# Optimization experiments

Hardware: AMD Instinct MI355X
Metric: run time of the kernel (lower is better)

## Reference

```python
import jax, jax.numpy as jnp
import numpy as np

BITS = 4
GROUP = 128
IN_F = 4096
OUT_F = 4096
N_TOK = 8192
N_STAGES = 4
QMAX = 2 ** BITS - 1  # affine (sym=False)


def _round_ste(x):
    return x + jax.lax.stop_gradient(jnp.round(x) - x)


def _clamp_ste(x, lo, hi):
    return x + jax.lax.stop_gradient(jnp.clip(x, lo, hi) - x)


def apply_rotation(x, pairs, theta, group_size):
    # x: [N, H]; pairs: [R, H] int (per-group index pairs in [0, group_size));
    # theta: [R, H//2]
    n, h = x.shape
    g = h // group_size
    half = group_size // 2
    offsets = (jnp.arange(g, dtype=jnp.int32) * group_size)[:, None]  # [G,1]
    pair_view = pairs.reshape(pairs.shape[0], g, half, 2)
    theta_view = theta.reshape(theta.shape[0], g, half)
    out = x
    for r in range(pairs.shape[0]):  # small fixed number of rotation stages
        idx_i = (pair_view[r, :, :, 0] + offsets).reshape(-1)  # [H//2]
        idx_j = (pair_view[r, :, :, 1] + offsets).reshape(-1)
        xi = out[:, idx_i]  # [N, H//2]
        xj = out[:, idx_j]
        c = jnp.cos(theta_view[r]).reshape(-1)[None, :]
        s = jnp.sin(theta_view[r]).reshape(-1)[None, :]
        out = out.at[:, idx_i].set(xi * c + xj * s).at[:, idx_j].set(-xi * s + xj * c)
    return out


def quant_dequant_affine_ste(w, scale, zero_point_float, group_size):
    # pseudo_quantize_dequant with sym=False, use_ste=True
    view = w.reshape(-1, group_size)
    s = _clamp_ste(scale, 1e-5, 1e5)
    rzp = _clamp_ste(-_round_ste(zero_point_float), 0.0, float(QMAX))
    q = _round_ste(view / s) + rzp
    q = _clamp_ste(q, 0.0, float(QMAX))
    return ((q - rzp) * s).reshape(w.shape)


def setup_inputs() -> dict:
    key = jax.random.key(0)
    k1, k2, k3, k4 = jax.random.split(key, 4)
    x = jax.random.normal(k1, (N_TOK, IN_F), dtype=jnp.float32)
    weight = jax.random.normal(k2, (OUT_F, IN_F), dtype=jnp.float32) * 0.02
    bias = jax.random.normal(k3, (OUT_F,), dtype=jnp.float32) * 0.01
    channel_scales = jnp.ones((IN_F,), dtype=jnp.float32)
    theta = jax.random.normal(k4, (N_STAGES, IN_F // 2), dtype=jnp.float32) * 0.05
    # per-group pair permutations: each stage/group is a permutation of [0, GROUP)
    rng = np.random.default_rng(0)
    g = IN_F // GROUP
    pairs_np = np.stack([
        np.concatenate([rng.permutation(GROUP) for _ in range(g)])
        for _ in range(N_STAGES)
    ]).astype(np.int32)  # [R, IN_F]
    pairs = jnp.asarray(pairs_np)
    # affine qparams from initial (theta=0, scales=1) transformed weight == weight
    view = weight.reshape(-1, GROUP)
    min_val = view.min(axis=1, keepdims=True)
    max_val = view.max(axis=1, keepdims=True)
    q_scale = jnp.clip(max_val - min_val, 1e-5, None) / QMAX
    q_zero_point = min_val / q_scale
    theta_mask = jnp.ones((N_STAGES, IN_F // 2), dtype=bool)
    return {"x": x, "weight": weight, "bias": bias,
            "channel_scales": channel_scales, "theta": theta,
            "q_scale": q_scale, "q_zero_point": q_zero_point,
            "pairs": pairs, "theta_mask": theta_mask}


def reference(x, weight, bias, channel_scales, theta, q_scale, q_zero_point, pairs, theta_mask):
    # transformed_weight(): scale input channels then group-wise Givens rotate
    w_scaled = weight * channel_scales[None, :]
    w_t = apply_rotation(w_scaled, pairs, theta, GROUP)
    # STE pseudo quantize-dequantize in the transformed domain
    w_q = quant_dequant_affine_ste(w_t, q_scale, q_zero_point, GROUP)
    # inverse rotation back to the original input domain, undo channel scales
    w_back = apply_rotation(w_q, pairs[::-1], -theta[::-1], GROUP) / channel_scales[None, :]
    return x @ w_back.T + bias[None, :]
```

## Files before the change

### kernel.cpp

```cpp
#include <hip/hip_runtime.h>
#include <hip/hip_bf16.h>
#include <math.h>

#define IN_F    4096
#define OUT_F   4096
#define N_TOK   8192
#define GROUP   128
#define NSTAGE  4
#define NPAIRS  2048
#define QMAXF   15.0

typedef unsigned short u16;
typedef __bf16 bf16x8 __attribute__((ext_vector_type(8)));
typedef float  f32x4  __attribute__((ext_vector_type(4)));

struct alignas(8) U16x4 { u16 x, y, z, w; };

__device__ __forceinline__ u16 f2bf(float f) {
    unsigned u = __float_as_uint(f);
    unsigned r = (u + 0x7fffu + ((u >> 16) & 1u)) >> 16;
    return (u16)r;
}

__device__ __forceinline__ void gl_lds16(const void* g, void* l) {
    __builtin_amdgcn_global_load_lds(
        (const __attribute__((address_space(1))) void*)g,
        (__attribute__((address_space(3))) void*)l,
        16, 0, 0);
}

__global__ void make_tabs(const float* __restrict__ theta,
                          double* __restrict__ ctab, double* __restrict__ stab) {
    int i = blockIdx.x * 256 + threadIdx.x;
    if (i < NSTAGE * NPAIRS) {
        double t = (double)theta[i];
        ctab[i] = cos(t);
        stab[i] = sin(t);
    }
}

__global__ __launch_bounds__(256) void build_w(
    const float* __restrict__ weight, const float* __restrict__ cs,
    const float* __restrict__ qs, const float* __restrict__ qzp,
    const int* __restrict__ pairs,
    const double* __restrict__ ctab, const double* __restrict__ stab,
    u16* __restrict__ wb) {
    __shared__ double gbuf[4][GROUP];
    const int wave = threadIdx.x >> 6, l = threadIdx.x & 63;
    const int task = blockIdx.x * 4 + wave;
    const int o = task >> 5, g = task & 31;
    double* gb = gbuf[wave];
    const int e0 = g * GROUP;

    float2 wv = *(const float2*)(weight + (size_t)o * IN_F + e0 + 2 * l);
    float2 cv = *(const float2*)(cs + e0 + 2 * l);
    gb[2 * l]     = (double)wv.x * (double)cv.x;
    gb[2 * l + 1] = (double)wv.y * (double)cv.y;
    __builtin_amdgcn_wave_barrier();

    const int2* prs = (const int2*)pairs;

    for (int r = 0; r < NSTAGE; ++r) {
        int2 p = prs[r * (IN_F / 2) + g * 64 + l];
        double c = ctab[r * NPAIRS + g * 64 + l];
        double s = stab[r * NPAIRS + g * 64 + l];
        double xi = gb[p.x], xj = gb[p.y];
        __builtin_amdgcn_wave_barrier();
        gb[p.x] =  xi * c + xj * s;
        gb[p.y] = -xi * s + xj * c;
        __builtin_amdgcn_wave_barrier();
    }

    {
        double s   = fmin(fmax((double)qs[o * 32 + g], 1e-5), 1e5);
        double rzp = fmin(fmax(-rint((double)qzp[o * 32 + g]), 0.0), QMAXF);
#pragma unroll
        for (int e = 2 * l; e <= 2 * l + 1; ++e) {
            double q = rint(gb[e] / s) + rzp;
            q = fmin(fmax(q, 0.0), QMAXF);
            gb[e] = (q - rzp) * s;
        }
        __builtin_amdgcn_wave_barrier();
    }

    for (int r = NSTAGE - 1; r >= 0; --r) {
        int2 p = prs[r * (IN_F / 2) + g * 64 + l];
        double c = ctab[r * NPAIRS + g * 64 + l];
        double s = stab[r * NPAIRS + g * 64 + l];
        double xi = gb[p.x], xj = gb[p.y];
        __builtin_amdgcn_wave_barrier();
        gb[p.x] = xi * c - xj * s;
        gb[p.y] = xi * s + xj * c;
        __builtin_amdgcn_wave_barrier();
    }

    unsigned lo = f2bf((float)(gb[2 * l]     / (double)cv.x));
    unsigned hi = f2bf((float)(gb[2 * l + 1] / (double)cv.y));
    *(unsigned*)(wb + (size_t)o * IN_F + e0 + 2 * l) = lo | (hi << 16);
}

__global__ void cast_x(const float* __restrict__ x, u16* __restrict__ xb) {
    size_t i = ((size_t)blockIdx.x * 256 + threadIdx.x) * 4;
    float4 v = *(const float4*)(x + i);
    U16x4 o;
    o.x = f2bf(v.x); o.y = f2bf(v.y); o.z = f2bf(v.z); o.w = f2bf(v.w);
    *(U16x4*)(xb + i) = o;
}

__global__ __launch_bounds__(512, 2) void gemm_bt(
    const u16* __restrict__ A, const u16* __restrict__ B,
    const float* __restrict__ bias, float* __restrict__ C) {
    constexpr int K = IN_F;
    constexpr int N = OUT_F;
    constexpr int NS = K / 32;
    __shared__ __align__(16) u16 As[4][256 * 32];
    __shared__ __align__(16) u16 Bs[4][256 * 32];

    const int tid  = threadIdx.x;
    const int wave = tid >> 6, lane = tid & 63;
    const int lrow = lane & 15, lq = lane >> 4;
    const int wm = wave >> 2, wn = wave & 3;

    const int wg = (blockIdx.x & 7) * 64 + (blockIdx.x >> 3);
    const int mt = wg & 31, nt = wg >> 5;
    const int m0 = mt * 256, n0 = nt * 256;

    const int srow = tid >> 2;
    const int gch  = (tid & 3) ^ ((tid >> 3) & 3);
    const u16* pA0 = A + (size_t)(m0 + srow) * K + gch * 8;
    const u16* pA1 = pA0 + (size_t)128 * K;
    const u16* pB0 = B + (size_t)(n0 + srow) * K + gch * 8;
    const u16* pB1 = pB0 + (size_t)128 * K;

#define STAGE(slot, s) do {                                         \
        const int ko_ = (s) * 32;                                   \
        gl_lds16(pA0 + ko_, &As[slot][wave * 512]);                 \
        gl_lds16(pA1 + ko_, &As[slot][4096 + wave * 512]);          \
        gl_lds16(pB0 + ko_, &Bs[slot][wave * 512]);                 \
        gl_lds16(pB1 + ko_, &Bs[slot][4096 + wave * 512]);          \
    } while (0)

    f32x4 acc[8][4];
#pragma unroll
    for (int i = 0; i < 8; ++i)
#pragma unroll
        for (int j = 0; j < 4; ++j) acc[i][j] = (f32x4){0.f, 0.f, 0.f, 0.f};

    STAGE(0, 0); STAGE(1, 1); STAGE(2, 2);

#define BODY(s, VMSTR, DO_STAGE) do {                                          \
        asm volatile("s_waitcnt " VMSTR);                                      \
        __builtin_amdgcn_s_barrier();                                          \
        asm volatile("" ::: "memory");                                         \
        const u16* as_ = As[(s) & 3];                                          \
        const u16* bs_ = Bs[(s) & 3];                                          \
        bf16x8 af[8], bf[4];                                                   \
        _Pragma("unroll")                                                      \
        for (int mi = 0; mi < 8; ++mi) {                                       \
            int ar = wm * 128 + mi * 16 + lrow;                                \
            af[mi] = *(const bf16x8*)&as_[ar * 32 +                            \
                                          (((lq ^ (ar >> 1)) & 3) << 3)];      \
        }                                                                      \
        _Pragma("unroll")                                                      \
        for (int nj = 0; nj < 4; ++nj) {                                       \
            int br = wn * 64 + nj * 16 + lrow;                                 \
            bf[nj] = *(const bf16x8*)&bs_[br * 32 +                            \
                                          (((lq ^ (br >> 1)) & 3) << 3)];      \
        }                                                                      \
        if (DO_STAGE) STAGE(((s) + 3) & 3, (s) + 3);                           \
        __builtin_amdgcn_s_setprio(1);                                         \
        _Pragma("unroll")                                                      \
        for (int mi = 0; mi < 8; ++mi)                                         \
            _Pragma("unroll")                                                  \
            for (int nj = 0; nj < 4; ++nj)                                     \
                acc[mi][nj] = __builtin_amdgcn_mfma_f32_16x16x32_bf16(         \
                    af[mi], bf[nj], acc[mi][nj], 0, 0, 0);                     \
        __builtin_amdgcn_s_setprio(0);                                         \
        asm volatile("" ::: "memory");                                         \
    } while (0)

    for (int s = 0; s < NS - 3; ++s)
        BODY(s, "vmcnt(8)", 1);
    BODY(NS - 3, "vmcnt(8)", 0);
    BODY(NS - 2, "vmcnt(4)", 0);
    BODY(NS - 1, "vmcnt(0)", 0);

#undef BODY
#undef STAGE

#pragma unroll
    for (int mi = 0; mi < 8; ++mi) {
        int rb = m0 + wm * 128 + mi * 16 + lq * 4;
#pragma unroll
        for (int nj = 0; nj < 4; ++nj) {
            int col = n0 + wn * 64 + nj * 16 + lrow;
            float bv = bias[col];
#pragma unroll
            for (int r = 0; r < 4; ++r)
                C[(size_t)(rb + r) * N + col] = acc[mi][nj][r] + bv;
        }
    }
}

extern "C" void kernel_launch(void* const* d_in, const int* in_sizes, int n_in,
                              void* d_out, int out_size, void* d_ws, size_t ws_size,
                              hipStream_t stream) {
    const float* x    = (const float*)d_in[0];
    const float* w    = (const float*)d_in[1];
    const float* bias = (const float*)d_in[2];
    const float* cs   = (const float*)d_in[3];
    const float* th   = (const float*)d_in[4];
    const float* qs   = (const float*)d_in[5];
    const float* qzp  = (const float*)d_in[6];
    const int*   pr   = (const int*)d_in[7];
    float* out = (float*)d_out;

    char* ws = (char*)d_ws;
    double* ctab = (double*)ws;
    double* stab = (double*)(ws + 65536);
    u16*    xb   = (u16*)(ws + 131072);
    u16*    wb   = (u16*)(ws + 131072 + (size_t)N_TOK * IN_F * 2);

    hipLaunchKernelGGL(make_tabs, dim3((NSTAGE * NPAIRS + 255) / 256), dim3(256),
                       0, stream, th, ctab, stab);
    hipLaunchKernelGGL(build_w, dim3(OUT_F * 32 / 4), dim3(256), 0, stream,
                       w, cs, qs, qzp, pr, ctab, stab, wb);
    hipLaunchKernelGGL(cast_x, dim3(N_TOK * IN_F / 4 / 256), dim3(256), 0, stream,
                       x, xb);
    hipLaunchKernelGGL(gemm_bt, dim3((N_TOK / 256) * (OUT_F / 256)), dim3(512),
                       0, stream, xb, wb, bias, out);
}
```

Baseline: 634.9 us.

## Restructure GEMM main loop into 64-wide K tiles with interleaved ping-pong phases

The bf16 GEMM now stages 256x64 K-tiles in a double-buffered LDS layout with an 8-way XOR swizzle, replacing the 4-deep 32-wide ring. Each K-group is split into four phases that alternate LDS fragment reads and MFMA bursts, separated by barriers. Global-to-LDS loads for A and B are issued at different phases so memory traffic overlaps compute. This aims to cut per-iteration barrier and waitcnt overhead and to schedule waves in a ping-pong pattern. In exchange there are many more barriers per tile and a shallower prefetch depth, which risks stalls.

```diff
diff --git a/kernel.cpp b/kernel.cpp
--- a/kernel.cpp
+++ b/kernel.cpp
@@ -27,6 +27,12 @@
         (const __attribute__((address_space(1))) void*)g,
         (__attribute__((address_space(3))) void*)l,
         16, 0, 0);
+}
+
+__device__ __forceinline__ void bar() {
+    asm volatile("" ::: "memory");
+    __builtin_amdgcn_s_barrier();
+    asm volatile("" ::: "memory");
 }
 
 __global__ void make_tabs(const float* __restrict__ theta,
@@ -112,9 +118,10 @@
     const float* __restrict__ bias, float* __restrict__ C) {
     constexpr int K = IN_F;
     constexpr int N = OUT_F;
-    constexpr int NS = K / 32;
-    __shared__ __align__(16) u16 As[4][256 * 32];
-    __shared__ __align__(16) u16 Bs[4][256 * 32];
+    constexpr int NGRP = K / 64;
+    constexpr int TIL = 256 * 64;
+    __shared__ __align__(16) u16 As[2][TIL];
+    __shared__ __align__(16) u16 Bs[2][TIL];
 
     const int tid  = threadIdx.x;
     const int wave = tid >> 6, lane = tid & 63;
@@ -125,19 +132,54 @@
     const int mt = wg & 31, nt = wg >> 5;
     const int m0 = mt * 256, n0 = nt * 256;
 
-    const int srow = tid >> 2;
-    const int gch  = (tid & 3) ^ ((tid >> 3) & 3);
-    const u16* pA0 = A + (size_t)(m0 + srow) * K + gch * 8;
-    const u16* pA1 = pA0 + (size_t)128 * K;
-    const u16* pB0 = B + (size_t)(n0 + srow) * K + gch * 8;
-    const u16* pB1 = pB0 + (size_t)128 * K;
-
-#define STAGE(slot, s) do {                                         \
-        const int ko_ = (s) * 32;                                   \
-        gl_lds16(pA0 + ko_, &As[slot][wave * 512]);                 \
-        gl_lds16(pA1 + ko_, &As[slot][4096 + wave * 512]);          \
-        gl_lds16(pB0 + ko_, &Bs[slot][wave * 512]);                 \
-        gl_lds16(pB1 + ko_, &Bs[slot][4096 + wave * 512]);          \
+    const int prow = tid >> 3;
+    const int pch  = (tid & 7) ^ ((tid >> 3) & 7);
+    const u16* pA = A + (size_t)(m0 + prow) * K + pch * 8;
+    const u16* pB = B + (size_t)(n0 + prow) * K + pch * 8;
+
+#define STAGE_A(slot, t) do {                                                  \
+        _Pragma("unroll")                                                      \
+        for (int hr_ = 0; hr_ < 4; ++hr_) {                                    \
+            const int h_ = hr_ >> 1, r_ = hr_ & 1;                             \
+            gl_lds16(pA + (size_t)(h_ * 128 + r_ * 64) * K + (t) * 64,         \
+                     &As[slot][h_ * 8192 + r_ * 4096 + (wave << 9)]);          \
+        }                                                                      \
+    } while (0)
+#define STAGE_B(slot, t) do {                                                  \
+        _Pragma("unroll")                                                      \
+        for (int hr_ = 0; hr_ < 4; ++hr_) {                                    \
+            const int h_ = hr_ >> 1, r_ = hr_ & 1;                             \
+            gl_lds16(pB + (size_t)(h_ * 128 + r_ * 64) * K + (t) * 64,         \
+                     &Bs[slot][h_ * 8192 + r_ * 4096 + (wave << 9)]);          \
+        }                                                                      \
+    } while (0)
+
+#define RD_A(ks) do {                                                          \
+        _Pragma("unroll")                                                      \
+        for (int mi_ = 0; mi_ < 8; ++mi_) {                                    \
+            const int ar_ = (wm << 7) + (mi_ << 4) + lrow;                     \
+            af[mi_] = *(const bf16x8*)&as_[(ar_ << 6) +                        \
+                (((((ks) << 2) | lq) ^ (ar_ & 7)) << 3)];                      \
+        }                                                                      \
+    } while (0)
+#define RD_B(ks, nj0) do {                                                     \
+        const int br0_ = (wn << 6) + ((nj0) << 4) + lrow;                      \
+        b0 = *(const bf16x8*)&bs_[(br0_ << 6) +                                \
+                (((((ks) << 2) | lq) ^ (br0_ & 7)) << 3)];                     \
+        b1 = *(const bf16x8*)&bs_[((br0_ + 16) << 6) +                         \
+                (((((ks) << 2) | lq) ^ (br0_ & 7)) << 3)];                     \
+    } while (0)
+
+#define MF2(nj0) do {                                                          \
+        __builtin_amdgcn_s_setprio(1);                                         \
+        _Pragma("unroll")                                                      \
+        for (int mi_ = 0; mi_ < 8; ++mi_) {                                    \
+            acc[mi_][nj0] = __builtin_amdgcn_mfma_f32_16x16x32_bf16(           \
+                af[mi_], b0, acc[mi_][nj0], 0, 0, 0);                          \
+            acc[mi_][(nj0) + 1] = __builtin_amdgcn_mfma_f32_16x16x32_bf16(     \
+                af[mi_], b1, acc[mi_][(nj0) + 1], 0, 0, 0);                    \
+        }                                                                      \
+        __builtin_amdgcn_s_setprio(0);                                         \
     } while (0)
 
     f32x4 acc[8][4];
@@ -146,47 +188,52 @@
 #pragma unroll
         for (int j = 0; j < 4; ++j) acc[i][j] = (f32x4){0.f, 0.f, 0.f, 0.f};
 
-    STAGE(0, 0); STAGE(1, 1); STAGE(2, 2);
-
-#define BODY(s, VMSTR, DO_STAGE) do {                                          \
-        asm volatile("s_waitcnt " VMSTR);                                      \
-        __builtin_amdgcn_s_barrier();                                          \
-        asm volatile("" ::: "memory");                                         \
-        const u16* as_ = As[(s) & 3];                                          \
-        const u16* bs_ = Bs[(s) & 3];                                          \
-        bf16x8 af[8], bf[4];                                                   \
-        _Pragma("unroll")                                                      \
-        for (int mi = 0; mi < 8; ++mi) {                                       \
-            int ar = wm * 128 + mi * 16 + lrow;                                \
-            af[mi] = *(const bf16x8*)&as_[ar * 32 +                            \
-                                          (((lq ^ (ar >> 1)) & 3) << 3)];      \
-        }                                                                      \
-        _Pragma("unroll")                                                      \
-        for (int nj = 0; nj < 4; ++nj) {                                       \
-            int br = wn * 64 + nj * 16 + lrow;                                 \
-            bf[nj] = *(const bf16x8*)&bs_[br * 32 +                            \
-                                          (((lq ^ (br >> 1)) & 3) << 3)];      \
-        }                                                                      \
-        if (DO_STAGE) STAGE(((s) + 3) & 3, (s) + 3);                           \
-        __builtin_amdgcn_s_setprio(1);                                         \
-        _Pragma("unroll")                                                      \
-        for (int mi = 0; mi < 8; ++mi)                                         \
-            _Pragma("unroll")                                                  \
-            for (int nj = 0; nj < 4; ++nj)                                     \
-                acc[mi][nj] = __builtin_amdgcn_mfma_f32_16x16x32_bf16(         \
-                    af[mi], bf[nj], acc[mi][nj], 0, 0, 0);                     \
-        __builtin_amdgcn_s_setprio(0);                                         \
-        asm volatile("" ::: "memory");                                         \
-    } while (0)
-
-    for (int s = 0; s < NS - 3; ++s)
-        BODY(s, "vmcnt(8)", 1);
-    BODY(NS - 3, "vmcnt(8)", 0);
-    BODY(NS - 2, "vmcnt(4)", 0);
-    BODY(NS - 1, "vmcnt(0)", 0);
-
-#undef BODY
-#undef STAGE
+    STAGE_A(0, 0); STAGE_B(0, 0); STAGE_A(1, 1); STAGE_B(1, 1);
+    asm volatile("s_waitcnt vmcnt(8)" ::: "memory");
+    __builtin_amdgcn_s_barrier();
+    asm volatile("" ::: "memory");
+
+#pragma unroll 2
+    for (int g = 0; g < NGRP; ++g) {
+        u16* as_ = As[g & 1];
+        u16* bs_ = Bs[g & 1];
+        bf16x8 af[8], b0, b1;
+
+        RD_A(0);
+        RD_B(0, 0);
+        if (g >= 1 && g + 1 < NGRP) STAGE_B((g + 1) & 1, g + 1);
+        bar();
+        MF2(0);
+        bar();
+
+        RD_B(0, 2);
+        bar();
+        MF2(2);
+        bar();
+
+        RD_A(1);
+        RD_B(1, 0);
+        bar();
+        MF2(0);
+        bar();
+
+        RD_B(1, 2);
+        if (g + 2 < NGRP) {
+            STAGE_A(g & 1, g + 2);
+            asm volatile("s_waitcnt vmcnt(4)" ::: "memory");
+        } else if (g + 1 < NGRP) {
+            asm volatile("s_waitcnt vmcnt(0)" ::: "memory");
+        }
+        bar();
+        MF2(2);
+        bar();
+    }
+
+#undef STAGE_A
+#undef STAGE_B
+#undef RD_A
+#undef RD_B
+#undef MF2
 
 #pragma unroll
     for (int mi = 0; mi < 8; ++mi) {
```

After: 672.6 us. 5.9% more time.
